# Kernel tuning notes

Measured on AMD Instinct MI355X. Metric: run time of the kernel, lower is better.

The kernel has to match this reference:

```python
import jax, jax.numpy as jnp
import numpy as np

B, S, D = 2, 2048, 1024
H, Hd = 16, 64
THD = H * Hd  # total_head_dim
LAMBDA_INIT = 0.8
ROPE_BASE = 10000.0
GN_EPS = 1e-5


def _rope_tables(seq_len, head_dim, dtype):
    inv_freq = 1.0 / (ROPE_BASE ** (jnp.arange(0, head_dim, 2, dtype=jnp.float32) / head_dim))
    t = jnp.arange(seq_len, dtype=jnp.float32)
    freqs = jnp.outer(t, inv_freq)                      # (S, Hd/2)
    emb = jnp.concatenate([freqs, freqs], axis=-1)      # (S, Hd)
    return jnp.cos(emb).astype(dtype), jnp.sin(emb).astype(dtype)


def _rotate_half(x):
    x1, x2 = jnp.split(x, 2, axis=-1)
    return jnp.concatenate([-x2, x1], axis=-1)


def _apply_rope(q, k, cos, sin):
    # q, k: (B, H, S, Hd); cos/sin: (S, Hd)
    cos = cos[None, None, :, :]
    sin = sin[None, None, :, :]
    q = q * cos + _rotate_half(q) * sin
    k = k * cos + _rotate_half(k) * sin
    return q, k


def setup_inputs() -> dict:
    key = jax.random.key(0)
    ks = jax.random.split(key, 8)
    s_in = 1.0 / np.sqrt(D)
    s_out = 1.0 / np.sqrt(THD)
    return {
        "x": jax.random.normal(ks[0], (B, S, D), dtype=jnp.float32),
        "Wq": jax.random.normal(ks[1], (D, 2 * THD), dtype=jnp.float32) * s_in,
        "Wk": jax.random.normal(ks[2], (D, 2 * THD), dtype=jnp.float32) * s_in,
        "Wv": jax.random.normal(ks[3], (D, THD), dtype=jnp.float32) * s_in,
        "Wo": jax.random.normal(ks[4], (THD, D), dtype=jnp.float32) * s_out,
        "lambda_q1": jnp.full((H,), LAMBDA_INIT, dtype=jnp.float32),
        "lambda_k1": jnp.full((H,), LAMBDA_INIT, dtype=jnp.float32),
        "lambda_q2": jnp.full((H,), LAMBDA_INIT, dtype=jnp.float32),
        "lambda_k2": jnp.full((H,), LAMBDA_INIT, dtype=jnp.float32),
        "lambda_init": jnp.asarray(LAMBDA_INIT, dtype=jnp.float32),
        "gn_weight": jnp.ones((THD,), dtype=jnp.float32),
        "gn_bias": jnp.zeros((THD,), dtype=jnp.float32),
    }


def reference(x, Wq, Wk, Wv, Wo, lambda_q1, lambda_k1, lambda_q2, lambda_k2,
              lambda_init, gn_weight, gn_bias):
    b, s, _ = x.shape
    scale = Hd ** -0.5

    q = (x @ Wq).reshape(b, s, 2, H, Hd).transpose(0, 2, 3, 1, 4)  # (B,2,H,S,Hd)
    k = (x @ Wk).reshape(b, s, 2, H, Hd).transpose(0, 2, 3, 1, 4)
    v = (x @ Wv).reshape(b, s, H, Hd).transpose(0, 2, 1, 3)        # (B,H,S,Hd)

    q1, q2 = q[:, 0], q[:, 1]
    k1, k2 = k[:, 0], k[:, 1]

    cos, sin = _rope_tables(s, Hd, x.dtype)
    q1, k1 = _apply_rope(q1, k1, cos, sin)
    q2, k2 = _apply_rope(q2, k2, cos, sin)

    attn1 = jax.nn.softmax(jnp.einsum("bhqd,bhkd->bhqk", q1, k1) * scale, axis=-1)
    attn2 = jax.nn.softmax(jnp.einsum("bhqd,bhkd->bhqk", q2, k2) * scale, axis=-1)

    lam1 = jnp.exp(lambda_q1 * lambda_k1).reshape(1, H, 1, 1)
    lam2 = jnp.exp(lambda_q2 * lambda_k2).reshape(1, H, 1, 1)
    lam_full = lam1 - lam2 + lambda_init

    attn_diff = attn1 - lam_full * attn2
    out = jnp.einsum("bhqk,bhkd->bhqd", attn_diff, v)              # (B,H,S,Hd)
    out = out.transpose(0, 2, 1, 3).reshape(b * s, H, Hd)           # (B*S,H,Hd)

    # GroupNorm with num_groups=H over channels THD: normalize each head's Hd
    mean = out.mean(axis=-1, keepdims=True)
    var = out.var(axis=-1, keepdims=True)
    out = (out - mean) * jax.lax.rsqrt(var + GN_EPS)
    out = out * gn_weight.reshape(H, Hd) + gn_bias.reshape(H, Hd)

    out = out.reshape(b, s, THD) * (1.0 - lambda_init)
    return out @ Wo
```

## Files before the change

### kernel.cpp

```cpp
#include <hip/hip_runtime.h>
#include <hip/hip_fp16.h>
#include <math.h>

#define NH     16
#define HD     64
#define S_LEN  2048
#define THD_   1024
#define SCALE_LOG2E 0.18033688011112042f

typedef __fp16 f16x8 __attribute__((ext_vector_type(8)));
typedef __fp16 f16x4 __attribute__((ext_vector_type(4)));
typedef __fp16 f16x2 __attribute__((ext_vector_type(2)));
typedef float  f32x4 __attribute__((ext_vector_type(4)));


__global__ __launch_bounds__(256) void wt_kernel(const float* __restrict__ W,
                                                 __half* __restrict__ WT,
                                                 int nmask, int nshift) {
  int id = blockIdx.x * 256 + threadIdx.x;
  int n = id & nmask;
  int k8 = (id >> nshift) * 8;
  int N = nmask + 1;
  f16x8 h;
#pragma unroll
  for (int j = 0; j < 8; ++j)
    h[j] = (__fp16)W[(size_t)(k8 + j) * N + n];
  *(f16x8*)(WT + (size_t)n * 1024 + k8) = h;
}

__global__ __launch_bounds__(256) void rope_tab_kernel(float2* __restrict__ tab) {
  int id = blockIdx.x * 256 + threadIdx.x;
  int p = id & 31;
  int s = id >> 5;
  float inv = expf(-0.28782313662425574f * (float)p);
  float sn, cs;
  sincosf((float)s * inv, &sn, &cs);
  tab[id] = make_float2(cs, sn);
}

template <int MODE>
__global__ __launch_bounds__(256) void mfma_gemm(const void* __restrict__ Ap,
                                                 const void* __restrict__ Bp,
                                                 void* __restrict__ Cp,
                                                 const float2* __restrict__ tab) {
  __shared__ __fp16 As[128][72];
  __shared__ __fp16 Bs[64][72];
  const int t = threadIdx.x;
  const int w = t >> 6, lane = t & 63;
  const int quad = lane >> 4, lqi = lane & 15;
  const int wm = w * 32;
  const int n0 = blockIdx.x * 64, m0 = blockIdx.y * 128;

  f32x4 acc[2][4];
#pragma unroll
  for (int mt = 0; mt < 2; ++mt)
#pragma unroll
    for (int nt = 0; nt < 4; ++nt) acc[mt][nt] = (f32x4){0.f, 0.f, 0.f, 0.f};

  const int srow = t >> 3;
  const int sc8 = (t & 7) * 8;
  const int gn_ = t & 63;
  const int gk0 = (t >> 6) * 8;

  for (int k0 = 0; k0 < 1024; k0 += 64) {
    if (k0) __syncthreads();
    if (MODE == 3) {
      const __half* A16 = (const __half*)Ap;
#pragma unroll
      for (int p = 0; p < 4; ++p) {
        int row = srow + 32 * p;
        *(f16x8*)&As[row][sc8] =
            *(const f16x8*)(A16 + (size_t)(m0 + row) * 1024 + k0 + sc8);
      }
    } else {
      const float* A32 = (const float*)Ap;
#pragma unroll
      for (int p = 0; p < 4; ++p) {
        int row = srow + 32 * p;
        const float* src = A32 + (size_t)(m0 + row) * 1024 + k0 + sc8;
        float4 u = *(const float4*)src;
        float4 v = *(const float4*)(src + 4);
        f16x8 h;
        h[0] = (__fp16)u.x; h[1] = (__fp16)u.y;
        h[2] = (__fp16)u.z; h[3] = (__fp16)u.w;
        h[4] = (__fp16)v.x; h[5] = (__fp16)v.y;
        h[6] = (__fp16)v.z; h[7] = (__fp16)v.w;
        *(f16x8*)&As[row][sc8] = h;
      }
    }
    if (MODE == 2) {
      const float* B32 = (const float*)Bp;
#pragma unroll
      for (int p = 0; p < 2; ++p) {
        int kc = gk0 + 32 * p;
        f16x8 h;
#pragma unroll
        for (int j = 0; j < 8; ++j)
          h[j] = (__fp16)B32[(size_t)(k0 + kc + j) * 1024 + n0 + gn_];
        *(f16x8*)&Bs[gn_][kc] = h;
      }
    } else {
      const __half* B16 = (const __half*)Bp;
      if (srow < 32) {
#pragma unroll
        for (int p = 0; p < 2; ++p) {
          int row = srow + 32 * p;
          *(f16x8*)&Bs[row][sc8] =
              *(const f16x8*)(B16 + (size_t)(n0 + row) * 1024 + k0 + sc8);
        }
      }
    }
    __syncthreads();
#pragma unroll
    for (int ks = 0; ks < 2; ++ks) {
      f16x8 af[2], bf[4];
#pragma unroll
      for (int mt = 0; mt < 2; ++mt)
        af[mt] = *(const f16x8*)&As[wm + mt * 16 + lqi][ks * 32 + quad * 8];
#pragma unroll
      for (int nt = 0; nt < 4; ++nt)
        bf[nt] = *(const f16x8*)&Bs[nt * 16 + lqi][ks * 32 + quad * 8];
#pragma unroll
      for (int mt = 0; mt < 2; ++mt)
#pragma unroll
        for (int nt = 0; nt < 4; ++nt)
          acc[mt][nt] = __builtin_amdgcn_mfma_f32_16x16x32_f16(
              af[mt], bf[nt], acc[mt][nt], 0, 0, 0);
    }
  }

  const int b = m0 >> 11;
  const int s0 = (m0 & 2047) + wm + quad * 4;
  if (MODE == 0) {
    __half* dst = (__half*)Cp;
    const int comp = n0 >> 10, hh = (n0 >> 6) & 15;
    __half* base = dst + ((size_t)(b * 2 + comp) * NH + hh) * (size_t)S_LEN * HD;
#pragma unroll
    for (int nt = 0; nt < 2; ++nt) {
      int p = nt * 16 + lqi;
#pragma unroll
      for (int mt = 0; mt < 2; ++mt) {
#pragma unroll
        for (int i = 0; i < 4; ++i) {
          int s = s0 + mt * 16 + i;
          float2 cs = tab[s * 32 + p];
          float x1 = acc[mt][nt][i], x2 = acc[mt][nt + 2][i];
          base[(size_t)s * HD + p] = __float2half(x1 * cs.x - x2 * cs.y);
          base[(size_t)s * HD + p + 32] = __float2half(x2 * cs.x + x1 * cs.y);
        }
      }
    }
  } else if (MODE == 2) {
    __half* vt = (__half*)Cp;
    const int hh = n0 >> 6;
#pragma unroll
    for (int nt = 0; nt < 4; ++nt) {
      int hd = nt * 16 + lqi;
      __half* base = vt + (((size_t)b * NH + hh) * HD + hd) * S_LEN;
#pragma unroll
      for (int mt = 0; mt < 2; ++mt) {
        f16x4 hv;
#pragma unroll
        for (int i = 0; i < 4; ++i) hv[i] = (__fp16)acc[mt][nt][i];
        *(f16x4*)(base + s0 + mt * 16) = hv;
      }
    }
  } else {
    float* Co = (float*)Cp;
#pragma unroll
    for (int mt = 0; mt < 2; ++mt)
#pragma unroll
      for (int i = 0; i < 4; ++i) {
        int m = m0 + wm + mt * 16 + quad * 4 + i;
#pragma unroll
        for (int nt = 0; nt < 4; ++nt)
          Co[(size_t)m * 1024 + n0 + nt * 16 + lqi] = acc[mt][nt][i];
      }
  }
}

__global__ __launch_bounds__(256, 2) void attn_kernel(
    const __half* __restrict__ q_h, const __half* __restrict__ k_h,
    const __half* __restrict__ vt_h, float* __restrict__ out,
    const float* __restrict__ lq1, const float* __restrict__ lk1,
    const float* __restrict__ lq2, const float* __restrict__ lk2,
    const float* __restrict__ lam_init_p) {
  __shared__ __half KV[24][512];
  __shared__ __half P_lds[4][2][32][72];

  const int t = threadIdx.x;
  const int w = t >> 6, lane = t & 63;
  const int quad = lane >> 4, lqi = lane & 15;
  const int qt = blockIdx.x;
  const int bh = blockIdx.y;
  const int b = bh >> 4, h = bh & 15;

  const size_t c1 = ((size_t)(b * 2 + 0) * NH + h) * (size_t)S_LEN * HD;
  const size_t c2 = ((size_t)(b * 2 + 1) * NH + h) * (size_t)S_LEN * HD;
  const size_t vtb = ((size_t)b * NH + h) * (size_t)HD * S_LEN;
  const int q0 = qt * 128 + w * 32;

  f16x8 qf[2][2][2];
#pragma unroll
  for (int nt = 0; nt < 2; ++nt)
#pragma unroll
    for (int ks = 0; ks < 2; ++ks) {
      size_t a = (size_t)(q0 + nt * 16 + lqi) * HD + ks * 32 + quad * 8;
      qf[0][nt][ks] = *(const f16x8*)(q_h + c1 + a);
      qf[1][nt][ks] = *(const f16x8*)(q_h + c2 + a);
    }

  f32x4 O[2][4][2];
#pragma unroll
  for (int s = 0; s < 2; ++s)
#pragma unroll
    for (int mt = 0; mt < 4; ++mt)
#pragma unroll
      for (int nt = 0; nt < 2; ++nt) O[s][mt][nt] = (f32x4){0.f, 0.f, 0.f, 0.f};
  float lsum[2][2] = {{0.f, 0.f}, {0.f, 0.f}};

  for (int kt = 0; kt < 32; ++kt) {
    const int k0 = kt * 64;
    __syncthreads();
#pragma unroll
    for (int ci = 0; ci < 6; ++ci) {
      const int c = w + ci * 4;
      const __half* g;
      if (c < 16) {
        int str = c >> 3, mt = (c >> 1) & 3, ks = c & 1;
        g = k_h + (str ? c2 : c1) +
            (size_t)(k0 + mt * 16 + lqi) * HD + ks * 32 + quad * 8;
      } else {
        int cc = c - 16;
        int ks2 = cc >> 2, mt = cc & 3;
        g = vt_h + vtb + (size_t)(mt * 16 + lqi) * S_LEN + k0 + ks2 * 32 +
            quad * 8;
      }
      *(f16x8*)&KV[c][lane * 8] = *(const f16x8*)g;
    }
    __syncthreads();

#pragma unroll
    for (int mt = 0; mt < 4; ++mt) {
#pragma unroll
      for (int str = 0; str < 2; ++str) {
        f16x8 kf0 = *(const f16x8*)&KV[str * 8 + mt * 2 + 0][lane * 8];
        f16x8 kf1 = *(const f16x8*)&KV[str * 8 + mt * 2 + 1][lane * 8];
#pragma unroll
        for (int nt = 0; nt < 2; ++nt) {
          f32x4 s = (f32x4){0.f, 0.f, 0.f, 0.f};
          s = __builtin_amdgcn_mfma_f32_16x16x32_f16(kf0, qf[str][nt][0], s,
                                                     0, 0, 0);
          s = __builtin_amdgcn_mfma_f32_16x16x32_f16(kf1, qf[str][nt][1], s,
                                                     0, 0, 0);
          float e0 = __builtin_amdgcn_exp2f(s[0] * SCALE_LOG2E);
          float e1 = __builtin_amdgcn_exp2f(s[1] * SCALE_LOG2E);
          float e2 = __builtin_amdgcn_exp2f(s[2] * SCALE_LOG2E);
          float e3 = __builtin_amdgcn_exp2f(s[3] * SCALE_LOG2E);
          lsum[str][nt] += (e0 + e1) + (e2 + e3);
          union { f16x4 v; f16x2 h2[2]; } pu;
          pu.h2[0] = __builtin_amdgcn_cvt_pkrtz(e0, e1);
          pu.h2[1] = __builtin_amdgcn_cvt_pkrtz(e2, e3);
          *(f16x4*)&P_lds[w][str][nt * 16 + lqi][mt * 16 + quad * 4] = pu.v;
        }
      }
    }
#pragma unroll
    for (int ks2 = 0; ks2 < 2; ++ks2) {
      f16x8 pf[2][2];
#pragma unroll
      for (int str = 0; str < 2; ++str)
#pragma unroll
        for (int nt = 0; nt < 2; ++nt)
          pf[str][nt] = *(const f16x8*)&P_lds[w][str][nt * 16 + lqi]
                                             [ks2 * 32 + quad * 8];
#pragma unroll
      for (int mt = 0; mt < 4; ++mt) {
        f16x8 vf = *(const f16x8*)&KV[16 + ks2 * 4 + mt][lane * 8];
#pragma unroll
        for (int str = 0; str < 2; ++str)
#pragma unroll
          for (int nt = 0; nt < 2; ++nt)
            O[str][mt][nt] = __builtin_amdgcn_mfma_f32_16x16x32_f16(
                vf, pf[str][nt], O[str][mt][nt], 0, 0, 0);
      }
    }
  }

  const float lam0 = lam_init_p[0];
  const float lam = expf(lq1[h] * lk1[h]) - expf(lq2[h] * lk2[h]) + lam0;
#pragma unroll
  for (int str = 0; str < 2; ++str)
#pragma unroll
    for (int nt = 0; nt < 2; ++nt) {
      float v = lsum[str][nt];
      v += __shfl_xor(v, 16);
      v += __shfl_xor(v, 32);
      lsum[str][nt] = v;
    }
#pragma unroll
  for (int nt = 0; nt < 2; ++nt) {
    float il1 = 1.f / lsum[0][nt];
    float il2 = lam / lsum[1][nt];
    int q = q0 + nt * 16 + lqi;
#pragma unroll
    for (int mt = 0; mt < 4; ++mt) {
      f32x4 o;
#pragma unroll
      for (int i = 0; i < 4; ++i)
        o[i] = O[0][mt][nt][i] * il1 - O[1][mt][nt][i] * il2;
      *(f32x4*)(out + ((size_t)(b * S_LEN + q)) * THD_ + h * HD + mt * 16 +
                quad * 4) = o;
    }
  }
}

__global__ __launch_bounds__(256) void gn_kernel(
    const float* __restrict__ src, __half* __restrict__ dst,
    const float* __restrict__ gw, const float* __restrict__ gb,
    const float* __restrict__ lam_init_p) {
  int g = blockIdx.x * 4 + (threadIdx.x >> 6);
  int lane = threadIdx.x & 63;
  float v = src[(size_t)g * 64 + lane];
  float s = v, sq = v * v;
#pragma unroll
  for (int off = 32; off; off >>= 1) {
    s += __shfl_xor(s, off);
    sq += __shfl_xor(sq, off);
  }
  float mean = s * (1.f / 64.f);
  float var = sq * (1.f / 64.f) - mean * mean;
  float rs = rsqrtf(var + 1e-5f);
  int h = g & 15;
  float w = gw[h * 64 + lane], bb = gb[h * 64 + lane];
  dst[(size_t)g * 64 + lane] =
      __float2half(((v - mean) * rs * w + bb) * (1.f - lam_init_p[0]));
}

extern "C" void kernel_launch(void* const* d_in, const int* in_sizes, int n_in,
                              void* d_out, int out_size, void* d_ws,
                              size_t ws_size, hipStream_t stream) {
  const float* x = (const float*)d_in[0];
  const float* Wq = (const float*)d_in[1];
  const float* Wk = (const float*)d_in[2];
  const float* Wv = (const float*)d_in[3];
  const float* Wo = (const float*)d_in[4];
  const float* lq1 = (const float*)d_in[5];
  const float* lk1 = (const float*)d_in[6];
  const float* lq2 = (const float*)d_in[7];
  const float* lk2 = (const float*)d_in[8];
  const float* lam_init = (const float*)d_in[9];
  const float* gnw = (const float*)d_in[10];
  const float* gnb = (const float*)d_in[11];
  float* out = (float*)d_out;

  __half* q_h = (__half*)d_ws;
  __half* k_h = q_h + 8388608;
  __half* vt_h = k_h + 8388608;
  __half* WqT = k_h;
  __half* WkT = vt_h;
  float2* tab = (float2*)(vt_h + 2097152);
  __half* WoT = q_h;
  __half* gn_h = q_h + 1048576;

  dim3 blk(256);
  wt_kernel<<<1024, blk, 0, stream>>>(Wq, WqT, 2047, 11);
  wt_kernel<<<1024, blk, 0, stream>>>(Wk, WkT, 2047, 11);
  rope_tab_kernel<<<256, blk, 0, stream>>>(tab);
  mfma_gemm<0><<<dim3(32, 32), blk, 0, stream>>>(x, WqT, q_h, tab);
  mfma_gemm<0><<<dim3(32, 32), blk, 0, stream>>>(x, WkT, k_h, tab);
  mfma_gemm<2><<<dim3(16, 32), blk, 0, stream>>>(x, Wv, vt_h, nullptr);
  attn_kernel<<<dim3(16, 32), blk, 0, stream>>>(q_h, k_h, vt_h, out, lq1, lk1,
                                                lq2, lk2, lam_init);
  wt_kernel<<<512, blk, 0, stream>>>(Wo, WoT, 1023, 10);
  gn_kernel<<<16384, blk, 0, stream>>>(out, gn_h, gnw, gnb, lam_init);
  mfma_gemm<3><<<dim3(16, 32), blk, 0, stream>>>(gn_h, WoT, out, nullptr);
}
```

Baseline: 338.8 us.

## Prefetch next K/V tile into registers and merge small prep kernels

The attention loop now loads the next K/V chunk from global memory into registers while the current tile is being computed, then stores it to shared memory at the top of the next iteration. This hides global load latency behind the MFMA work. Separately, the Wq/Wk transposes and the rope table are combined into one launch, and the Wo transpose is folded into the groupnorm kernel, cutting kernel launch count. The prefetch costs six extra vector registers per thread, which may affect occupancy.

```diff
diff --git a/kernel.cpp b/kernel.cpp
--- a/kernel.cpp
+++ b/kernel.cpp
@@ -14,10 +14,9 @@
 typedef float  f32x4 __attribute__((ext_vector_type(4)));
 
 
-__global__ __launch_bounds__(256) void wt_kernel(const float* __restrict__ W,
-                                                 __half* __restrict__ WT,
-                                                 int nmask, int nshift) {
-  int id = blockIdx.x * 256 + threadIdx.x;
+__device__ inline void wt_body(const float* __restrict__ W,
+                               __half* __restrict__ WT, int id, int nmask,
+                               int nshift) {
   int n = id & nmask;
   int k8 = (id >> nshift) * 8;
   int N = nmask + 1;
@@ -28,14 +27,25 @@
   *(f16x8*)(WT + (size_t)n * 1024 + k8) = h;
 }
 
-__global__ __launch_bounds__(256) void rope_tab_kernel(float2* __restrict__ tab) {
-  int id = blockIdx.x * 256 + threadIdx.x;
-  int p = id & 31;
-  int s = id >> 5;
-  float inv = expf(-0.28782313662425574f * (float)p);
-  float sn, cs;
-  sincosf((float)s * inv, &sn, &cs);
-  tab[id] = make_float2(cs, sn);
+__global__ __launch_bounds__(256) void prep_kernel(
+    const float* __restrict__ Wq, const float* __restrict__ Wk,
+    __half* __restrict__ WqT, __half* __restrict__ WkT,
+    float2* __restrict__ tab) {
+  int bid = blockIdx.x;
+  int t = threadIdx.x;
+  if (bid < 1024) {
+    wt_body(Wq, WqT, bid * 256 + t, 2047, 11);
+  } else if (bid < 2048) {
+    wt_body(Wk, WkT, (bid - 1024) * 256 + t, 2047, 11);
+  } else {
+    int id = (bid - 2048) * 256 + t;
+    int p = id & 31;
+    int s = id >> 5;
+    float inv = expf(-0.28782313662425574f * (float)p);
+    float sn, cs;
+    sincosf((float)s * inv, &sn, &cs);
+    tab[id] = make_float2(cs, sn);
+  }
 }
 
 template <int MODE>
@@ -219,26 +229,34 @@
       for (int nt = 0; nt < 2; ++nt) O[s][mt][nt] = (f32x4){0.f, 0.f, 0.f, 0.f};
   float lsum[2][2] = {{0.f, 0.f}, {0.f, 0.f}};
 
+  auto chunk_addr = [&](int c, int k0) -> const __half* {
+    if (c < 16) {
+      int str = c >> 3, mt = (c >> 1) & 3, ks = c & 1;
+      return k_h + (str ? c2 : c1) + (size_t)(k0 + mt * 16 + lqi) * HD +
+             ks * 32 + quad * 8;
+    }
+    int cc = c - 16, ks2 = cc >> 2, mt = cc & 3;
+    return vt_h + vtb + (size_t)(mt * 16 + lqi) * S_LEN + k0 + ks2 * 32 +
+           quad * 8;
+  };
+
+  f16x8 r[6];
+#pragma unroll
+  for (int ci = 0; ci < 6; ++ci)
+    r[ci] = *(const f16x8*)chunk_addr(w + ci * 4, 0);
+
   for (int kt = 0; kt < 32; ++kt) {
-    const int k0 = kt * 64;
+    if (kt) __syncthreads();
+#pragma unroll
+    for (int ci = 0; ci < 6; ++ci)
+      *(f16x8*)&KV[w + ci * 4][lane * 8] = r[ci];
     __syncthreads();
-#pragma unroll
-    for (int ci = 0; ci < 6; ++ci) {
-      const int c = w + ci * 4;
-      const __half* g;
-      if (c < 16) {
-        int str = c >> 3, mt = (c >> 1) & 3, ks = c & 1;
-        g = k_h + (str ? c2 : c1) +
-            (size_t)(k0 + mt * 16 + lqi) * HD + ks * 32 + quad * 8;
-      } else {
-        int cc = c - 16;
-        int ks2 = cc >> 2, mt = cc & 3;
-        g = vt_h + vtb + (size_t)(mt * 16 + lqi) * S_LEN + k0 + ks2 * 32 +
-            quad * 8;
-      }
-      *(f16x8*)&KV[c][lane * 8] = *(const f16x8*)g;
-    }
-    __syncthreads();
+
+    if (kt < 31) {
+#pragma unroll
+      for (int ci = 0; ci < 6; ++ci)
+        r[ci] = *(const f16x8*)chunk_addr(w + ci * 4, (kt + 1) * 64);
+    }
 
 #pragma unroll
     for (int mt = 0; mt < 4; ++mt) {
@@ -315,10 +333,15 @@
   }
 }
 
-__global__ __launch_bounds__(256) void gn_kernel(
+__global__ __launch_bounds__(256) void gn_wt_kernel(
     const float* __restrict__ src, __half* __restrict__ dst,
     const float* __restrict__ gw, const float* __restrict__ gb,
-    const float* __restrict__ lam_init_p) {
+    const float* __restrict__ lam_init_p, const float* __restrict__ Wo,
+    __half* __restrict__ WoT) {
+  if (blockIdx.x >= 16384) {
+    wt_body(Wo, WoT, (blockIdx.x - 16384) * 256 + threadIdx.x, 1023, 10);
+    return;
+  }
   int g = blockIdx.x * 4 + (threadIdx.x >> 6);
   int lane = threadIdx.x & 63;
   float v = src[(size_t)g * 64 + lane];
@@ -364,15 +387,13 @@
   __half* gn_h = q_h + 1048576;
 
   dim3 blk(256);
-  wt_kernel<<<1024, blk, 0, stream>>>(Wq, WqT, 2047, 11);
-  wt_kernel<<<1024, blk, 0, stream>>>(Wk, WkT, 2047, 11);
-  rope_tab_kernel<<<256, blk, 0, stream>>>(tab);
+  prep_kernel<<<2304, blk, 0, stream>>>(Wq, Wk, WqT, WkT, tab);
   mfma_gemm<0><<<dim3(32, 32), blk, 0, stream>>>(x, WqT, q_h, tab);
   mfma_gemm<0><<<dim3(32, 32), blk, 0, stream>>>(x, WkT, k_h, tab);
   mfma_gemm<2><<<dim3(16, 32), blk, 0, stream>>>(x, Wv, vt_h, nullptr);
   attn_kernel<<<dim3(16, 32), blk, 0, stream>>>(q_h, k_h, vt_h, out, lq1, lk1,
                                                 lq2, lk2, lam_init);
-  wt_kernel<<<512, blk, 0, stream>>>(Wo, WoT, 1023, 10);
-  gn_kernel<<<16384, blk, 0, stream>>>(out, gn_h, gnw, gnb, lam_init);
+  gn_wt_kernel<<<16896, blk, 0, stream>>>(out, gn_h, gnw, gnb, lam_init, Wo,
+                                          WoT);
   mfma_gemm<3><<<dim3(16, 32), blk, 0, stream>>>(gn_h, WoT, out, nullptr);
 }
```

Result: faster. 331.4 us (-2.2%).
